# Kernel optimization log

Measured on AMD Instinct MI355X. Metric: run time of the kernel, lower is better.

## Reference

```python
import jax, jax.numpy as jnp
import numpy as np

DELTA = 0.0          # init kwarg (torch default is 0.7; 0.0 used so random data selects pairs)
N, T = 1_048_576, 32  # samples x trait columns
COS_EPS = 1e-8       # torch.cosine_similarity eps


def setup_inputs() -> dict:
    key = jax.random.key(0)
    k1, k2 = jax.random.split(key)
    return {
        "y_pred": jax.random.normal(k1, (N, T), dtype=jnp.float32),
        "y_true": jax.random.normal(k2, (N, T), dtype=jnp.float32),
    }


def reference(y_pred, y_true):
    t = y_true.shape[1]
    # Pearson correlation matrix over columns of y_true (centered Gram + norm outer)
    xc = y_true - jnp.mean(y_true, axis=0, keepdims=True)      # [N, T]
    nx = jnp.sqrt(jnp.sum(xc * xc, axis=0))                    # [T]
    pcc = jnp.einsum('nj,nk->jk', xc, xc) / (nx[:, None] * nx[None, :])
    # Cosine similarity matrix over columns of y_pred
    pn = jnp.sqrt(jnp.sum(y_pred * y_pred, axis=0))            # [T]
    denom = jnp.maximum(pn[:, None] * pn[None, :], COS_EPS)
    cos = jnp.einsum('nj,nk->jk', y_pred, y_pred) / denom      # [T, T]
    # Pair mask: 1 <= j < k < T (loop starts at j=1 in the original)
    idx = jnp.arange(t)
    pair_mask = (idx[None, :] > idx[:, None]) & (idx[:, None] >= 1)
    sel = pair_mask & (pcc >= DELTA)
    c = (t - 1) * (t - 2) // 2                                 # total pair count (incl. unselected)
    total = jnp.sum(jnp.where(sel, 1.0 - cos, 0.0))
    return total / c
```

## Files before the change

kernel.cpp:

```cpp
#include <hip/hip_runtime.h>

#define N_ROWS   1048576
#define T_COLS   32
#define NBLK     1024
#define BLOCK    256
#define RSTAGE   128
#define STAGES   8
#define ROWSTR   72
#define PRED_OFF 36
#define NWS      2080

__global__ __launch_bounds__(256) void ts_zero(float* __restrict__ ws) {
    for (int i = threadIdx.x; i < NWS; i += 256) ws[i] = 0.0f;
}

__global__ __launch_bounds__(256, 4) void ts_gram(const float* __restrict__ y_pred,
                                                  const float* __restrict__ y_true,
                                                  float* __restrict__ ws) {
    __shared__ __align__(16) float s_data[RSTAGE * ROWSTR];

    const int tid = threadIdx.x;
    const int g   = tid >> 5;
    const int tau = tid & 31;
    const int mtx = tau >> 4;
    const int tt  = tau & 15;
    const int j0  = (tt >> 2) * 8;
    const int k0  = (tt & 3) * 8;
    const int moff = mtx * PRED_OFF;

    float acc[8][8];
    #pragma unroll
    for (int a = 0; a < 8; ++a)
        #pragma unroll
        for (int b = 0; b < 8; ++b) acc[a][b] = 0.0f;
    float sumv[8];
    #pragma unroll
    for (int a = 0; a < 8; ++a) sumv[a] = 0.0f;

    const size_t row0 = (size_t)blockIdx.x * (N_ROWS / NBLK);

    for (int s = 0; s < STAGES; ++s) {
        const float4* gt = (const float4*)(y_true + (row0 + (size_t)s * RSTAGE) * T_COLS);
        const float4* gp = (const float4*)(y_pred + (row0 + (size_t)s * RSTAGE) * T_COLS);
        __syncthreads();
        #pragma unroll
        for (int i = 0; i < 4; ++i) {
            int f  = tid + i * 256;
            int r  = f >> 3;
            int c4 = (f & 7) * 4;
            *(float4*)(s_data + r * ROWSTR + c4)            = gt[f];
            *(float4*)(s_data + r * ROWSTR + PRED_OFF + c4) = gp[f];
        }
        __syncthreads();

        const float* base = s_data + moff;
        #pragma unroll 2
        for (int rr = 0; rr < 16; ++rr) {
            const float* row = base + (g * 16 + rr) * ROWSTR;
            float4 a0 = *(const float4*)(row + j0);
            float4 a1 = *(const float4*)(row + j0 + 4);
            float4 b0 = *(const float4*)(row + k0);
            float4 b1 = *(const float4*)(row + k0 + 4);
            float aj[8] = {a0.x, a0.y, a0.z, a0.w, a1.x, a1.y, a1.z, a1.w};
            float bk[8] = {b0.x, b0.y, b0.z, b0.w, b1.x, b1.y, b1.z, b1.w};
            #pragma unroll
            for (int jj = 0; jj < 8; ++jj)
                #pragma unroll
                for (int kk = 0; kk < 8; ++kk)
                    acc[jj][kk] = fmaf(aj[jj], bk[kk], acc[jj][kk]);
            if (mtx == 0) {
                #pragma unroll
                for (int jj = 0; jj < 8; ++jj) sumv[jj] += aj[jj];
            }
        }
    }

    __syncthreads();
    for (int i = tid; i < NWS; i += 256) s_data[i] = 0.0f;
    __syncthreads();
    #pragma unroll
    for (int jj = 0; jj < 8; ++jj)
        #pragma unroll
        for (int kk = 0; kk < 8; ++kk)
            atomicAdd(&s_data[mtx * 1024 + (j0 + jj) * 32 + (k0 + kk)], acc[jj][kk]);
    if (mtx == 0 && k0 == 0) {
        #pragma unroll
        for (int jj = 0; jj < 8; ++jj) atomicAdd(&s_data[2048 + j0 + jj], sumv[jj]);
    }
    __syncthreads();
    for (int i = tid; i < NWS; i += 256) atomicAdd(&ws[i], s_data[i]);
}

__global__ __launch_bounds__(1024) void ts_final(const float* __restrict__ w,
                                                 float* __restrict__ out) {
    __shared__ float s_S[32], s_nx[32], s_pn[32];
    __shared__ float s_red[16];
    const int tid = threadIdx.x;
    const float invN = 1.0f / (float)N_ROWS;

    if (tid < 32) {
        float S = w[2048 + tid];
        s_S[tid] = S;
        float d = w[tid * 32 + tid] - S * S * invN;
        s_nx[tid] = sqrtf(d);
        s_pn[tid] = sqrtf(w[1024 + tid * 33]);
    }
    __syncthreads();

    const int j = tid >> 5, k = tid & 31;
    float contrib = 0.0f;
    if (j >= 1 && k > j) {
        float gc  = w[j * 32 + k] - s_S[j] * s_S[k] * invN;
        float pcc = gc / (s_nx[j] * s_nx[k]);
        float cs  = w[1024 + j * 32 + k] / fmaxf(s_pn[j] * s_pn[k], 1e-8f);
        if (pcc >= 0.0f) contrib = 1.0f - cs;
    }
    #pragma unroll
    for (int off = 32; off > 0; off >>= 1) contrib += __shfl_down(contrib, off);
    if ((tid & 63) == 0) s_red[tid >> 6] = contrib;
    __syncthreads();
    if (tid == 0) {
        float tot = 0.0f;
        #pragma unroll
        for (int i = 0; i < 16; ++i) tot += s_red[i];
        out[0] = tot * (1.0f / 465.0f);
    }
}

extern "C" void kernel_launch(void* const* d_in, const int* in_sizes, int n_in,
                              void* d_out, int out_size, void* d_ws, size_t ws_size,
                              hipStream_t stream) {
    const float* y_pred = (const float*)d_in[0];
    const float* y_true = (const float*)d_in[1];
    float* out = (float*)d_out;
    float* ws  = (float*)d_ws;

    ts_zero<<<1, 256, 0, stream>>>(ws);
    ts_gram<<<NBLK, BLOCK, 0, stream>>>(y_pred, y_true, ws);
    ts_final<<<1, 1024, 0, stream>>>(ws, out);
}
```

Measured before the change: 365.1 us.

## Read rows directly from global memory instead of staging through LDS

Drops the shared-memory staging loop with its two barriers per stage. Each thread group now reads its own contiguous row slice straight from global memory using float4 loads that hit cache. The grid doubles to 2048 blocks and the zero-init kernel becomes a hipMemsetAsync. In exchange, global atomic traffic doubles with the block count, and the 16 lanes working on the same matrix all load the same row, which relies on L1/L2 to absorb the redundant reads.

```diff
diff --git a/kernel.cpp b/kernel.cpp
--- a/kernel.cpp
+++ b/kernel.cpp
@@ -2,22 +2,16 @@
 
 #define N_ROWS   1048576
 #define T_COLS   32
-#define NBLK     1024
+#define NBLK     2048
 #define BLOCK    256
-#define RSTAGE   128
-#define STAGES   8
-#define ROWSTR   72
-#define PRED_OFF 36
+#define ROWS_PER_BLK  (N_ROWS / NBLK)
+#define ROWS_PER_GRP  (ROWS_PER_BLK / 8)
 #define NWS      2080
-
-__global__ __launch_bounds__(256) void ts_zero(float* __restrict__ ws) {
-    for (int i = threadIdx.x; i < NWS; i += 256) ws[i] = 0.0f;
-}
 
 __global__ __launch_bounds__(256, 4) void ts_gram(const float* __restrict__ y_pred,
                                                   const float* __restrict__ y_true,
                                                   float* __restrict__ ws) {
-    __shared__ __align__(16) float s_data[RSTAGE * ROWSTR];
+    __shared__ float s_red[NWS];
 
     const int tid = threadIdx.x;
     const int g   = tid >> 5;
@@ -26,7 +20,10 @@
     const int tt  = tau & 15;
     const int j0  = (tt >> 2) * 8;
     const int k0  = (tt & 3) * 8;
-    const int moff = mtx * PRED_OFF;
+
+    const float* src = mtx ? y_pred : y_true;
+    const size_t row0 = (size_t)blockIdx.x * ROWS_PER_BLK + (size_t)g * ROWS_PER_GRP;
+    const float* p = src + row0 * T_COLS;
 
     float acc[8][8];
     #pragma unroll
@@ -37,58 +34,39 @@
     #pragma unroll
     for (int a = 0; a < 8; ++a) sumv[a] = 0.0f;
 
-    const size_t row0 = (size_t)blockIdx.x * (N_ROWS / NBLK);
-
-    for (int s = 0; s < STAGES; ++s) {
-        const float4* gt = (const float4*)(y_true + (row0 + (size_t)s * RSTAGE) * T_COLS);
-        const float4* gp = (const float4*)(y_pred + (row0 + (size_t)s * RSTAGE) * T_COLS);
-        __syncthreads();
+    #pragma unroll 4
+    for (int r = 0; r < ROWS_PER_GRP; ++r) {
+        const float* row = p + r * T_COLS;
+        float4 a0 = *(const float4*)(row + j0);
+        float4 a1 = *(const float4*)(row + j0 + 4);
+        float4 b0 = *(const float4*)(row + k0);
+        float4 b1 = *(const float4*)(row + k0 + 4);
+        float aj[8] = {a0.x, a0.y, a0.z, a0.w, a1.x, a1.y, a1.z, a1.w};
+        float bk[8] = {b0.x, b0.y, b0.z, b0.w, b1.x, b1.y, b1.z, b1.w};
         #pragma unroll
-        for (int i = 0; i < 4; ++i) {
-            int f  = tid + i * 256;
-            int r  = f >> 3;
-            int c4 = (f & 7) * 4;
-            *(float4*)(s_data + r * ROWSTR + c4)            = gt[f];
-            *(float4*)(s_data + r * ROWSTR + PRED_OFF + c4) = gp[f];
-        }
-        __syncthreads();
-
-        const float* base = s_data + moff;
-        #pragma unroll 2
-        for (int rr = 0; rr < 16; ++rr) {
-            const float* row = base + (g * 16 + rr) * ROWSTR;
-            float4 a0 = *(const float4*)(row + j0);
-            float4 a1 = *(const float4*)(row + j0 + 4);
-            float4 b0 = *(const float4*)(row + k0);
-            float4 b1 = *(const float4*)(row + k0 + 4);
-            float aj[8] = {a0.x, a0.y, a0.z, a0.w, a1.x, a1.y, a1.z, a1.w};
-            float bk[8] = {b0.x, b0.y, b0.z, b0.w, b1.x, b1.y, b1.z, b1.w};
+        for (int jj = 0; jj < 8; ++jj)
             #pragma unroll
-            for (int jj = 0; jj < 8; ++jj)
-                #pragma unroll
-                for (int kk = 0; kk < 8; ++kk)
-                    acc[jj][kk] = fmaf(aj[jj], bk[kk], acc[jj][kk]);
-            if (mtx == 0) {
-                #pragma unroll
-                for (int jj = 0; jj < 8; ++jj) sumv[jj] += aj[jj];
-            }
+            for (int kk = 0; kk < 8; ++kk)
+                acc[jj][kk] = fmaf(aj[jj], bk[kk], acc[jj][kk]);
+        if (mtx == 0) {
+            #pragma unroll
+            for (int jj = 0; jj < 8; ++jj) sumv[jj] += aj[jj];
         }
     }
 
-    __syncthreads();
-    for (int i = tid; i < NWS; i += 256) s_data[i] = 0.0f;
+    for (int i = tid; i < NWS; i += BLOCK) s_red[i] = 0.0f;
     __syncthreads();
     #pragma unroll
     for (int jj = 0; jj < 8; ++jj)
         #pragma unroll
         for (int kk = 0; kk < 8; ++kk)
-            atomicAdd(&s_data[mtx * 1024 + (j0 + jj) * 32 + (k0 + kk)], acc[jj][kk]);
+            atomicAdd(&s_red[mtx * 1024 + (j0 + jj) * 32 + (k0 + kk)], acc[jj][kk]);
     if (mtx == 0 && k0 == 0) {
         #pragma unroll
-        for (int jj = 0; jj < 8; ++jj) atomicAdd(&s_data[2048 + j0 + jj], sumv[jj]);
+        for (int jj = 0; jj < 8; ++jj) atomicAdd(&s_red[2048 + j0 + jj], sumv[jj]);
     }
     __syncthreads();
-    for (int i = tid; i < NWS; i += 256) atomicAdd(&ws[i], s_data[i]);
+    for (int i = tid; i < NWS; i += BLOCK) atomicAdd(&ws[i], s_red[i]);
 }
 
 __global__ __launch_bounds__(1024) void ts_final(const float* __restrict__ w,
@@ -135,7 +113,7 @@
     float* out = (float*)d_out;
     float* ws  = (float*)d_ws;
 
-    ts_zero<<<1, 256, 0, stream>>>(ws);
+    hipMemsetAsync(ws, 0, NWS * sizeof(float), stream);
     ts_gram<<<NBLK, BLOCK, 0, stream>>>(y_pred, y_true, ws);
     ts_final<<<1, 1024, 0, stream>>>(ws, out);
 }
```

Result: slower. 620.7 us (+70.0%).
